# Kernel tuning notes

Hardware: AMD Instinct MI355X
Metric: run time of the kernel (lower is better)

## Reference

```python
import jax, jax.numpy as jnp
import numpy as np

N_NODES = 100000


def _graph_conv(x, src, dst, W, b):
    # DGL GraphConv, norm='both':
    # out = D_in^{-1/2} A D_out^{-1/2} x W + b, degrees clamped >= 1
    ones = jnp.ones(src.shape[0], dtype=x.dtype)
    deg_out = jax.ops.segment_sum(ones, src, num_segments=N_NODES)
    deg_in = jax.ops.segment_sum(ones, dst, num_segments=N_NODES)
    norm_src = jax.lax.rsqrt(jnp.maximum(deg_out, 1.0))  # [N]
    norm_dst = jax.lax.rsqrt(jnp.maximum(deg_in, 1.0))   # [N]
    h = x * norm_src[:, None]                    # [N, d_in]
    msg = h[src]                                 # [E, d_in] gather
    agg = jax.ops.segment_sum(msg, dst, num_segments=N_NODES)  # [N, d_in] scatter-add
    agg = agg * norm_dst[:, None]
    return agg @ W + b                           # [N, d_out]


def setup_inputs() -> dict:
    key = jax.random.key(0)
    k1, k2, k3, k4, k5 = jax.random.split(key, 5)
    n_edges = 1600000
    ndim, hdl, r = 32, 64, 32
    x = jax.random.normal(k1, (N_NODES, ndim), dtype=jnp.float32)
    src = jax.random.randint(k2, (n_edges,), 0, N_NODES, dtype=jnp.int32)
    dst = jax.random.randint(k3, (n_edges,), 0, N_NODES, dtype=jnp.int32)
    W1 = jax.random.normal(k4, (ndim, hdl), dtype=jnp.float32) / np.sqrt(ndim)
    b1 = jnp.zeros((hdl,), dtype=jnp.float32)
    W2 = jax.random.normal(k5, (hdl, r), dtype=jnp.float32) / np.sqrt(hdl)
    b2 = jnp.zeros((r,), dtype=jnp.float32)
    return {"x": x, "src": src, "dst": dst, "W1": W1, "b1": b1, "W2": W2, "b2": b2}


def reference(x, src, dst, W1, b1, W2, b2):
    z = _graph_conv(x, src, dst, W1, b1)
    z = _graph_conv(z, src, dst, W2, b2)
    return z
```

## Files before the change

### kernel.cpp

```cpp
#include <hip/hip_runtime.h>

#define N_NODES 100000
#define D_IN 32
#define D_HID 64
#define D_OUT 32
#define NBUCK 391
#define CHUNK 8192
#define CAP   8192

#define RED3(a) { a += __shfl_xor(a, 8); a += __shfl_xor(a, 16); a += __shfl_xor(a, 32); }

__global__ __launch_bounds__(256) void bucket_hist_kernel(
    const int* __restrict__ src, const int* __restrict__ dst,
    int* __restrict__ sb_cnt, int* __restrict__ db_cnt, int E) {
    __shared__ int hs[NBUCK], hd[NBUCK];
    int tid = threadIdx.x;
    for (int i = tid; i < NBUCK; i += 256) { hs[i] = 0; hd[i] = 0; }
    __syncthreads();
    int stride = gridDim.x * 256;
    for (int e = blockIdx.x * 256 + tid; e < E; e += stride) {
        atomicAdd(&hs[src[e] >> 8], 1);
        atomicAdd(&hd[dst[e] >> 8], 1);
    }
    __syncthreads();
    for (int i = tid; i < NBUCK; i += 256) {
        if (hs[i]) atomicAdd(&sb_cnt[i], hs[i]);
        if (hd[i]) atomicAdd(&db_cnt[i], hd[i]);
    }
}

__global__ __launch_bounds__(512) void bucket_scan_kernel(
    const int* __restrict__ sb_cnt, const int* __restrict__ db_cnt,
    int* __restrict__ sb_base, int* __restrict__ db_base,
    int* __restrict__ sb_cur, int* __restrict__ db_cur, int E) {
    __shared__ int s[512];
    int tid = threadIdx.x;
    int v = (tid < NBUCK) ? sb_cnt[tid] : 0;
    s[tid] = v;
    __syncthreads();
    for (int off = 1; off < 512; off <<= 1) {
        int tv = (tid >= off) ? s[tid - off] : 0;
        __syncthreads(); s[tid] += tv; __syncthreads();
    }
    if (tid < NBUCK) { int e0 = s[tid] - v; sb_base[tid] = e0; sb_cur[tid] = e0; }
    if (tid == 0) sb_base[NBUCK] = E;
    __syncthreads();
    int v2 = (tid < NBUCK) ? db_cnt[tid] : 0;
    s[tid] = v2;
    __syncthreads();
    for (int off = 1; off < 512; off <<= 1) {
        int tv = (tid >= off) ? s[tid - off] : 0;
        __syncthreads(); s[tid] += tv; __syncthreads();
    }
    if (tid < NBUCK) { int e0 = s[tid] - v2; db_base[tid] = e0; db_cur[tid] = e0; }
    if (tid == 0) db_base[NBUCK] = E;
}

__global__ __launch_bounds__(512) void partition_both_kernel(
    const int* __restrict__ src, const int* __restrict__ dst,
    int* __restrict__ sb_cur, int* __restrict__ db_cur,
    int* __restrict__ ebuf, unsigned char* __restrict__ sbuf, int E) {
    __shared__ int dh[NBUCK], sh_[NBUCK];
    __shared__ int sarr[512];
    __shared__ int dloff[NBUCK], dgb[NBUCK], dcur[NBUCK];
    __shared__ int sloff[NBUCK], sgb[NBUCK], scur[NBUCK];
    __shared__ int dbuf[CHUNK];
    __shared__ unsigned char sbytes[CHUNK];
    int tid = threadIdx.x;
    int base = blockIdx.x * CHUNK;
    int lim = E - base; if (lim > CHUNK) lim = CHUNK;

    for (int i = tid; i < NBUCK; i += 512) { dh[i] = 0; sh_[i] = 0; }
    __syncthreads();
    for (int k = tid; k < lim; k += 512) {
        atomicAdd(&dh[dst[base + k] >> 8], 1);
        atomicAdd(&sh_[src[base + k] >> 8], 1);
    }
    __syncthreads();
    int v = (tid < NBUCK) ? dh[tid] : 0;
    sarr[tid] = v;
    __syncthreads();
    for (int off = 1; off < 512; off <<= 1) {
        int tv = (tid >= off) ? sarr[tid - off] : 0;
        __syncthreads(); sarr[tid] += tv; __syncthreads();
    }
    if (tid < NBUCK) {
        int excl = sarr[tid] - v;
        dloff[tid] = excl; dcur[tid] = excl;
        dgb[tid] = v ? atomicAdd(&db_cur[tid], v) : 0;
    }
    __syncthreads();
    int v2 = (tid < NBUCK) ? sh_[tid] : 0;
    sarr[tid] = v2;
    __syncthreads();
    for (int off = 1; off < 512; off <<= 1) {
        int tv = (tid >= off) ? sarr[tid - off] : 0;
        __syncthreads(); sarr[tid] += tv; __syncthreads();
    }
    if (tid < NBUCK) {
        int excl = sarr[tid] - v2;
        sloff[tid] = excl; scur[tid] = excl;
        sgb[tid] = v2 ? atomicAdd(&sb_cur[tid], v2) : 0;
    }
    __syncthreads();
    for (int k = tid; k < lim; k += 512) {
        int d = dst[base + k], s0 = src[base + k];
        int p = atomicAdd(&dcur[d >> 8], 1);
        dbuf[p] = (s0 << 8) | (d & 255);
        int p2 = atomicAdd(&scur[s0 >> 8], 1);
        sbytes[p2] = (unsigned char)(s0 & 255);
    }
    __syncthreads();
    int w = tid >> 6, lane = tid & 63;
    for (int b = w; b < NBUCK; b += 8) {
        int st = dloff[b], len = dh[b], gb = dgb[b];
        for (int i = lane; i < len; i += 64) ebuf[gb + i] = dbuf[st + i];
        int st2 = sloff[b], len2 = sh_[b], gb2 = sgb[b];
        for (int i = lane; i < len2; i += 64) sbuf[gb2 + i] = sbytes[st2 + i];
    }
}

__global__ __launch_bounds__(256) void src_norm_prescale_kernel(
    const unsigned char* __restrict__ sbuf, const int* __restrict__ sb_base,
    const float4* __restrict__ x4, float4* __restrict__ xs4,
    float* __restrict__ norm_src, int n_nodes) {
    __shared__ int cnt[256];
    __shared__ float nsl[256];
    int b = blockIdx.x, tid = threadIdx.x;
    int st = sb_base[b], en = sb_base[b + 1];
    cnt[tid] = 0;
    __syncthreads();
    for (int k = st + tid; k < en; k += 256) atomicAdd(&cnt[sbuf[k]], 1);
    __syncthreads();
    int base_node = b << 8;
    int nn = n_nodes - base_node; if (nn > 256) nn = 256;
    if (tid < nn) {
        int d = cnt[tid];
        float ns = rsqrtf((float)(d < 1 ? 1 : d));
        norm_src[base_node + tid] = ns;
        nsl[tid] = ns;
    }
    __syncthreads();
    for (int k = tid; k < nn * 8; k += 256) {
        float4 v = x4[((long)base_node << 3) + k];
        float s = nsl[k >> 3];
        v.x *= s; v.y *= s; v.z *= s; v.w *= s;
        xs4[((long)base_node << 3) + k] = v;
    }
}

__global__ __launch_bounds__(256) void localfill_kernel(
    const int* __restrict__ ebuf, const int* __restrict__ db_base,
    int* __restrict__ rowptr, float* __restrict__ norm_dst,
    int* __restrict__ colidx, int n_nodes, int E) {
    __shared__ int limg[CAP];
    __shared__ int cnt[256];
    __shared__ int sc[256];
    int b = blockIdx.x, tid = threadIdx.x;
    int base_node = b << 8;
    int nn = n_nodes - base_node; if (nn > 256) nn = 256;
    int cbase = db_base[b], cend = db_base[b + 1];
    int len = cend - cbase;
    cnt[tid] = 0;
    __syncthreads();
    for (int k = tid; k < len; k += 256) atomicAdd(&cnt[ebuf[cbase + k] & 255], 1);
    __syncthreads();
    int v = cnt[tid];
    sc[tid] = v;
    __syncthreads();
    for (int off = 1; off < 256; off <<= 1) {
        int tv = (tid >= off) ? sc[tid - off] : 0;
        __syncthreads(); sc[tid] += tv; __syncthreads();
    }
    int excl = sc[tid] - v;
    if (tid < nn) {
        rowptr[base_node + tid] = cbase + excl;
        norm_dst[base_node + tid] = rsqrtf((float)(v < 1 ? 1 : v));
    }
    if (b == NBUCK - 1 && tid == 0) rowptr[n_nodes] = E;
    __syncthreads();
    cnt[tid] = excl;
    __syncthreads();
    if (len <= CAP) {
        for (int k = tid; k < len; k += 256) {
            int v2 = ebuf[cbase + k];
            int p = atomicAdd(&cnt[v2 & 255], 1);
            limg[p] = v2 >> 8;
        }
        __syncthreads();
        for (int k = tid; k < len; k += 256) colidx[cbase + k] = limg[k];
    } else {
        for (int k = tid; k < len; k += 256) {
            int v2 = ebuf[cbase + k];
            int p = atomicAdd(&cnt[v2 & 255], 1);
            colidx[cbase + p] = v2 >> 8;
        }
    }
}

__global__ __launch_bounds__(256) void layer1_fused(
    const float4* __restrict__ xs4, const int* __restrict__ colidx,
    const int* __restrict__ rowptr, const float* __restrict__ norm_src,
    const float* __restrict__ norm_dst,
    const float* __restrict__ W1, const float* __restrict__ b1,
    const float* __restrict__ W2, float* __restrict__ y, int n_nodes) {
    __shared__ float W1s[D_IN * D_HID];
    __shared__ float W2s[D_HID * D_OUT];
    __shared__ float b1s[D_HID];
    __shared__ float accs[4][2][D_IN];
    __shared__ float z1s[4][2][D_HID];
    int t = threadIdx.x;
    for (int i = t; i < D_IN * D_HID; i += 256) { W1s[i] = W1[i]; W2s[i] = W2[i]; }
    if (t < D_HID) b1s[t] = b1[t];
    __syncthreads();

    int w = t >> 6, lane = t & 63;
    int eh = lane >> 3;
    int q  = lane & 7;
    int j  = lane & 31;
    int half = lane >> 5;
    int npairs = (n_nodes + 1) >> 1;

    for (int p = blockIdx.x * 4 + w; p < npairs; p += gridDim.x * 4) {
        int nA = p * 2, nB = nA + 1;
        bool hasB = nB < n_nodes;
        int sA = rowptr[nA], eA = rowptr[nA + 1];
        int sB = hasB ? rowptr[nB] : 0, eB = hasB ? rowptr[nB + 1] : 0;
        int dA = eA - sA, dB = eB - sB;
        int dmax = dA > dB ? dA : dB;
        float aAx = 0.f, aAy = 0.f, aAz = 0.f, aAw = 0.f;
        float aBx = 0.f, aBy = 0.f, aBz = 0.f, aBw = 0.f;
        for (int base = 0; base < dmax; base += 64) {
            int limA = dA - base; limA = limA < 0 ? 0 : (limA > 64 ? 64 : limA);
            int limB = dB - base; limB = limB < 0 ? 0 : (limB > 64 ? 64 : limB);
            int cA = (lane < limA) ? colidx[sA + base + lane] : 0;
            int cB = (lane < limB) ? colidx[sB + base + lane] : 0;
            int lm = limA > limB ? limA : limB;
            int lim_up = (lm + 7) & ~7;
            for (int i = eh; i < lim_up; i += 8) {
                int ca = __shfl(cA, i), cb = __shfl(cB, i);
                if (i < limA) {
                    float4 v = xs4[(long)ca * 8 + q];
                    aAx += v.x; aAy += v.y; aAz += v.z; aAw += v.w;
                }
                if (i < limB) {
                    float4 v = xs4[(long)cb * 8 + q];
                    aBx += v.x; aBy += v.y; aBz += v.z; aBw += v.w;
                }
            }
        }
        RED3(aAx) RED3(aAy) RED3(aAz) RED3(aAw)
        RED3(aBx) RED3(aBy) RED3(aBz) RED3(aBw)
        if (lane < 16) {
            int s = lane >> 3, qq = lane & 7;
            accs[w][s][qq * 4 + 0] = s ? aBx : aAx;
            accs[w][s][qq * 4 + 1] = s ? aBy : aAy;
            accs[w][s][qq * 4 + 2] = s ? aBz : aAz;
            accs[w][s][qq * 4 + 3] = s ? aBw : aAw;
        }
        float ndA = norm_dst[nA], ndB = hasB ? norm_dst[nB] : 0.f;
        float s1A = 0.f, s1B = 0.f;
#pragma unroll
        for (int k = 0; k < D_IN; ++k) {
            float wv = W1s[k * D_HID + lane];
            s1A = fmaf(accs[w][0][k], wv, s1A);
            s1B = fmaf(accs[w][1][k], wv, s1B);
        }
        z1s[w][0][lane] = ndA * s1A + b1s[lane];
        z1s[w][1][lane] = ndB * s1B + b1s[lane];
        float s2 = 0.f;
#pragma unroll
        for (int k = 0; k < D_HID; ++k) s2 = fmaf(z1s[w][half][k], W2s[k * D_OUT + j], s2);
        int nn_ = half ? nB : nA;
        if (half == 0 || hasB) y[(long)nn_ * D_OUT + j] = norm_src[nn_] * s2;
    }
}

__global__ __launch_bounds__(256) void agg2_kernel(
    const float4* __restrict__ y4, const int* __restrict__ colidx,
    const int* __restrict__ rowptr, const float* __restrict__ norm_dst,
    const float* __restrict__ b2, float4* __restrict__ out4, int n_nodes) {
    int t = threadIdx.x;
    int w = t >> 6, lane = t & 63;
    int eh = lane >> 3, q = lane & 7;
    int npairs = (n_nodes + 1) >> 1;
    for (int p = blockIdx.x * 4 + w; p < npairs; p += gridDim.x * 4) {
        int nA = p * 2, nB = nA + 1;
        bool hasB = nB < n_nodes;
        int sA = rowptr[nA], eA = rowptr[nA + 1];
        int sB = hasB ? rowptr[nB] : 0, eB = hasB ? rowptr[nB + 1] : 0;
        int dA = eA - sA, dB = eB - sB;
        int dmax = dA > dB ? dA : dB;
        float aAx = 0.f, aAy = 0.f, aAz = 0.f, aAw = 0.f;
        float aBx = 0.f, aBy = 0.f, aBz = 0.f, aBw = 0.f;
        for (int base = 0; base < dmax; base += 64) {
            int limA = dA - base; limA = limA < 0 ? 0 : (limA > 64 ? 64 : limA);
            int limB = dB - base; limB = limB < 0 ? 0 : (limB > 64 ? 64 : limB);
            int cA = (lane < limA) ? colidx[sA + base + lane] : 0;
            int cB = (lane < limB) ? colidx[sB + base + lane] : 0;
            int lm = limA > limB ? limA : limB;
            int lim_up = (lm + 7) & ~7;
            for (int i = eh; i < lim_up; i += 8) {
                int ca = __shfl(cA, i), cb = __shfl(cB, i);
                if (i < limA) {
                    float4 v = y4[(long)ca * 8 + q];
                    aAx += v.x; aAy += v.y; aAz += v.z; aAw += v.w;
                }
                if (i < limB) {
                    float4 v = y4[(long)cb * 8 + q];
                    aBx += v.x; aBy += v.y; aBz += v.z; aBw += v.w;
                }
            }
        }
        RED3(aAx) RED3(aAy) RED3(aAz) RED3(aAw)
        RED3(aBx) RED3(aBy) RED3(aBz) RED3(aBw)
        if (lane < 16) {
            int s = lane >> 3;
            int nn_ = s ? nB : nA;
            if (!s || hasB) {
                float nd = norm_dst[nn_];
                const float4 bb = ((const float4*)b2)[q];
                float4 o;
                o.x = fmaf(s ? aBx : aAx, nd, bb.x);
                o.y = fmaf(s ? aBy : aAy, nd, bb.y);
                o.z = fmaf(s ? aBz : aAz, nd, bb.z);
                o.w = fmaf(s ? aBw : aAw, nd, bb.w);
                out4[(long)nn_ * 8 + q] = o;
            }
        }
    }
}

extern "C" void kernel_launch(void* const* d_in, const int* in_sizes, int n_in,
                              void* d_out, int out_size, void* d_ws, size_t ws_size,
                              hipStream_t stream) {
    const float* x   = (const float*)d_in[0];
    const int*   src = (const int*)d_in[1];
    const int*   dst = (const int*)d_in[2];
    const float* W1  = (const float*)d_in[3];
    const float* b1  = (const float*)d_in[4];
    const float* W2  = (const float*)d_in[5];
    const float* b2  = (const float*)d_in[6];

    const int N = N_NODES;
    const int E = in_sizes[1];

    int* ws_i    = (int*)d_ws;
    int* sb_cnt  = ws_i;
    int* db_cnt  = ws_i + 512;
    int* sb_base = ws_i + 1024;
    int* db_base = ws_i + 1536;
    int* sb_cur  = ws_i + 2048;
    int* db_cur  = ws_i + 2560;
    int* rowptr  = ws_i + 3072;
    int* colidx  = ws_i + 3072 + N + 4;
    float* norms = (float*)(colidx + E);
    float* yv    = norms + 2 * N;
    float* xs    = yv + 32 * N;
    int* ebuf    = (int*)yv;
    unsigned char* sbuf = (unsigned char*)(ebuf + E);

    hipMemsetAsync(ws_i, 0, 1024 * sizeof(int), stream);

    bucket_hist_kernel<<<256, 256, 0, stream>>>(src, dst, sb_cnt, db_cnt, E);
    bucket_scan_kernel<<<1, 512, 0, stream>>>(sb_cnt, db_cnt, sb_base, db_base,
                                              sb_cur, db_cur, E);

    int pb = (E + CHUNK - 1) / CHUNK;
    partition_both_kernel<<<pb, 512, 0, stream>>>(src, dst, sb_cur, db_cur,
                                                  ebuf, sbuf, E);
    src_norm_prescale_kernel<<<NBUCK, 256, 0, stream>>>(sbuf, sb_base,
                                                        (const float4*)x, (float4*)xs,
                                                        norms, N);
    localfill_kernel<<<NBUCK, 256, 0, stream>>>(ebuf, db_base, rowptr, norms + N,
                                                colidx, N, E);

    layer1_fused<<<2048, 256, 0, stream>>>((const float4*)xs, colidx, rowptr,
                                           norms, norms + N, W1, b1, W2, yv, N);
    agg2_kernel<<<2048, 256, 0, stream>>>((const float4*)yv, colidx, rowptr,
                                          norms + N, b2, (float4*)d_out, N);
}
```

Baseline: 194.7 us.

## Store gathered node features in bf16 and process one node per wavefront

The prescaled input features and the layer-1 output rows are now stored as bf16, which halves the bytes moved by the random row gathers in both aggregation kernels. Each wavefront now handles a single node with 16 edges in flight and 8 features per lane, where it previously interleaved two nodes. Rounding to bf16 adds error that may approach the correctness tolerance. The workspace layout is rearranged so the bf16 buffers alias the edge staging buffers.

```diff
diff --git a/kernel.cpp b/kernel.cpp
--- a/kernel.cpp
+++ b/kernel.cpp
@@ -8,7 +8,19 @@
 #define CHUNK 8192
 #define CAP   8192
 
-#define RED3(a) { a += __shfl_xor(a, 8); a += __shfl_xor(a, 16); a += __shfl_xor(a, 32); }
+typedef unsigned short ushort8v __attribute__((ext_vector_type(8)));
+typedef unsigned short ushort4v __attribute__((ext_vector_type(4)));
+
+__device__ __forceinline__ float bf2f(unsigned short u) {
+    return __uint_as_float((unsigned)u << 16);
+}
+__device__ __forceinline__ unsigned short f2bf(float f) {
+    unsigned u = __float_as_uint(f);
+    return (unsigned short)((u + 0x7FFF + ((u >> 16) & 1)) >> 16);
+}
+
+#define RED4(a) { a += __shfl_xor(a, 4); a += __shfl_xor(a, 8); \
+                  a += __shfl_xor(a, 16); a += __shfl_xor(a, 32); }
 
 __global__ __launch_bounds__(256) void bucket_hist_kernel(
     const int* __restrict__ src, const int* __restrict__ dst,
@@ -122,7 +134,7 @@
 
 __global__ __launch_bounds__(256) void src_norm_prescale_kernel(
     const unsigned char* __restrict__ sbuf, const int* __restrict__ sb_base,
-    const float4* __restrict__ x4, float4* __restrict__ xs4,
+    const float4* __restrict__ x4, ushort4v* __restrict__ xs4b,
     float* __restrict__ norm_src, int n_nodes) {
     __shared__ int cnt[256];
     __shared__ float nsl[256];
@@ -144,8 +156,10 @@
     for (int k = tid; k < nn * 8; k += 256) {
         float4 v = x4[((long)base_node << 3) + k];
         float s = nsl[k >> 3];
-        v.x *= s; v.y *= s; v.z *= s; v.w *= s;
-        xs4[((long)base_node << 3) + k] = v;
+        ushort4v o;
+        o[0] = f2bf(v.x * s); o[1] = f2bf(v.y * s);
+        o[2] = f2bf(v.z * s); o[3] = f2bf(v.w * s);
+        xs4b[((long)base_node << 3) + k] = o;
     }
 }
 
@@ -199,134 +213,110 @@
 }
 
 __global__ __launch_bounds__(256) void layer1_fused(
-    const float4* __restrict__ xs4, const int* __restrict__ colidx,
+    const ushort8v* __restrict__ xs8, const int* __restrict__ colidx,
     const int* __restrict__ rowptr, const float* __restrict__ norm_src,
     const float* __restrict__ norm_dst,
     const float* __restrict__ W1, const float* __restrict__ b1,
-    const float* __restrict__ W2, float* __restrict__ y, int n_nodes) {
+    const float* __restrict__ W2, unsigned short* __restrict__ ybf, int n_nodes) {
     __shared__ float W1s[D_IN * D_HID];
     __shared__ float W2s[D_HID * D_OUT];
     __shared__ float b1s[D_HID];
-    __shared__ float accs[4][2][D_IN];
-    __shared__ float z1s[4][2][D_HID];
+    __shared__ float accs[4][D_IN];
+    __shared__ float z1s[4][D_HID];
     int t = threadIdx.x;
-    for (int i = t; i < D_IN * D_HID; i += 256) { W1s[i] = W1[i]; W2s[i] = W2[i]; }
+    for (int i = t; i < 2048; i += 256) { W1s[i] = W1[i]; W2s[i] = W2[i]; }
     if (t < D_HID) b1s[t] = b1[t];
     __syncthreads();
 
     int w = t >> 6, lane = t & 63;
-    int eh = lane >> 3;
-    int q  = lane & 7;
+    int eh = lane >> 2;
+    int q  = lane & 3;
     int j  = lane & 31;
-    int half = lane >> 5;
-    int npairs = (n_nodes + 1) >> 1;
-
-    for (int p = blockIdx.x * 4 + w; p < npairs; p += gridDim.x * 4) {
-        int nA = p * 2, nB = nA + 1;
-        bool hasB = nB < n_nodes;
-        int sA = rowptr[nA], eA = rowptr[nA + 1];
-        int sB = hasB ? rowptr[nB] : 0, eB = hasB ? rowptr[nB + 1] : 0;
-        int dA = eA - sA, dB = eB - sB;
-        int dmax = dA > dB ? dA : dB;
-        float aAx = 0.f, aAy = 0.f, aAz = 0.f, aAw = 0.f;
-        float aBx = 0.f, aBy = 0.f, aBz = 0.f, aBw = 0.f;
-        for (int base = 0; base < dmax; base += 64) {
-            int limA = dA - base; limA = limA < 0 ? 0 : (limA > 64 ? 64 : limA);
-            int limB = dB - base; limB = limB < 0 ? 0 : (limB > 64 ? 64 : limB);
-            int cA = (lane < limA) ? colidx[sA + base + lane] : 0;
-            int cB = (lane < limB) ? colidx[sB + base + lane] : 0;
-            int lm = limA > limB ? limA : limB;
-            int lim_up = (lm + 7) & ~7;
-            for (int i = eh; i < lim_up; i += 8) {
-                int ca = __shfl(cA, i), cb = __shfl(cB, i);
-                if (i < limA) {
-                    float4 v = xs4[(long)ca * 8 + q];
-                    aAx += v.x; aAy += v.y; aAz += v.z; aAw += v.w;
-                }
-                if (i < limB) {
-                    float4 v = xs4[(long)cb * 8 + q];
-                    aBx += v.x; aBy += v.y; aBz += v.z; aBw += v.w;
+    int kb = (lane >> 5) * 32;
+
+    for (int n = blockIdx.x * 4 + w; n < n_nodes; n += gridDim.x * 4) {
+        int start = rowptr[n], deg = rowptr[n + 1] - start;
+        float a[8];
+#pragma unroll
+        for (int r = 0; r < 8; ++r) a[r] = 0.f;
+        for (int base = 0; base < deg; base += 64) {
+            int rem = deg - base;
+            int lim = rem < 64 ? rem : 64;
+            int lim_up = (lim + 15) & ~15;
+            int c_reg = (lane < lim) ? colidx[start + base + lane] : 0;
+            for (int i = eh; i < lim_up; i += 16) {
+                int c = __shfl(c_reg, i);
+                if (i < lim) {
+                    ushort8v v = xs8[(long)c * 4 + q];
+#pragma unroll
+                    for (int r = 0; r < 8; ++r) a[r] += bf2f(v[r]);
                 }
             }
         }
-        RED3(aAx) RED3(aAy) RED3(aAz) RED3(aAw)
-        RED3(aBx) RED3(aBy) RED3(aBz) RED3(aBw)
-        if (lane < 16) {
-            int s = lane >> 3, qq = lane & 7;
-            accs[w][s][qq * 4 + 0] = s ? aBx : aAx;
-            accs[w][s][qq * 4 + 1] = s ? aBy : aAy;
-            accs[w][s][qq * 4 + 2] = s ? aBz : aAz;
-            accs[w][s][qq * 4 + 3] = s ? aBw : aAw;
-        }
-        float ndA = norm_dst[nA], ndB = hasB ? norm_dst[nB] : 0.f;
-        float s1A = 0.f, s1B = 0.f;
-#pragma unroll
-        for (int k = 0; k < D_IN; ++k) {
-            float wv = W1s[k * D_HID + lane];
-            s1A = fmaf(accs[w][0][k], wv, s1A);
-            s1B = fmaf(accs[w][1][k], wv, s1B);
-        }
-        z1s[w][0][lane] = ndA * s1A + b1s[lane];
-        z1s[w][1][lane] = ndB * s1B + b1s[lane];
+#pragma unroll
+        for (int r = 0; r < 8; ++r) RED4(a[r])
+        if (lane < 4) {
+#pragma unroll
+            for (int r = 0; r < 8; ++r) accs[w][lane * 8 + r] = a[r];
+        }
+        float nd = norm_dst[n];
+        float s1 = 0.f;
+#pragma unroll
+        for (int k = 0; k < D_IN; ++k) s1 = fmaf(accs[w][k], W1s[k * D_HID + lane], s1);
+        z1s[w][lane] = nd * s1 + b1s[lane];
         float s2 = 0.f;
 #pragma unroll
-        for (int k = 0; k < D_HID; ++k) s2 = fmaf(z1s[w][half][k], W2s[k * D_OUT + j], s2);
-        int nn_ = half ? nB : nA;
-        if (half == 0 || hasB) y[(long)nn_ * D_OUT + j] = norm_src[nn_] * s2;
+        for (int kk = 0; kk < 32; ++kk) s2 = fmaf(z1s[w][kb + kk], W2s[(kb + kk) * D_OUT + j], s2);
+        s2 += __shfl_xor(s2, 32);
+        if (lane < 32) ybf[(long)n * D_OUT + j] = f2bf(norm_src[n] * s2);
     }
 }
 
 __global__ __launch_bounds__(256) void agg2_kernel(
-    const float4* __restrict__ y4, const int* __restrict__ colidx,
+    const ushort8v* __restrict__ y8, const int* __restrict__ colidx,
     const int* __restrict__ rowptr, const float* __restrict__ norm_dst,
-    const float* __restrict__ b2, float4* __restrict__ out4, int n_nodes) {
+    const float* __restrict__ b2, float* __restrict__ out, int n_nodes) {
+    __shared__ float b2s[D_OUT];
     int t = threadIdx.x;
+    if (t < D_OUT) b2s[t] = b2[t];
+    __syncthreads();
     int w = t >> 6, lane = t & 63;
-    int eh = lane >> 3, q = lane & 7;
-    int npairs = (n_nodes + 1) >> 1;
-    for (int p = blockIdx.x * 4 + w; p < npairs; p += gridDim.x * 4) {
-        int nA = p * 2, nB = nA + 1;
-        bool hasB = nB < n_nodes;
-        int sA = rowptr[nA], eA = rowptr[nA + 1];
-        int sB = hasB ? rowptr[nB] : 0, eB = hasB ? rowptr[nB + 1] : 0;
-        int dA = eA - sA, dB = eB - sB;
-        int dmax = dA > dB ? dA : dB;
-        float aAx = 0.f, aAy = 0.f, aAz = 0.f, aAw = 0.f;
-        float aBx = 0.f, aBy = 0.f, aBz = 0.f, aBw = 0.f;
-        for (int base = 0; base < dmax; base += 64) {
-            int limA = dA - base; limA = limA < 0 ? 0 : (limA > 64 ? 64 : limA);
-            int limB = dB - base; limB = limB < 0 ? 0 : (limB > 64 ? 64 : limB);
-            int cA = (lane < limA) ? colidx[sA + base + lane] : 0;
-            int cB = (lane < limB) ? colidx[sB + base + lane] : 0;
-            int lm = limA > limB ? limA : limB;
-            int lim_up = (lm + 7) & ~7;
-            for (int i = eh; i < lim_up; i += 8) {
-                int ca = __shfl(cA, i), cb = __shfl(cB, i);
-                if (i < limA) {
-                    float4 v = y4[(long)ca * 8 + q];
-                    aAx += v.x; aAy += v.y; aAz += v.z; aAw += v.w;
-                }
-                if (i < limB) {
-                    float4 v = y4[(long)cb * 8 + q];
-                    aBx += v.x; aBy += v.y; aBz += v.z; aBw += v.w;
+    int eh = lane >> 2, q = lane & 3;
+    for (int n = blockIdx.x * 4 + w; n < n_nodes; n += gridDim.x * 4) {
+        int start = rowptr[n], deg = rowptr[n + 1] - start;
+        float a[8];
+#pragma unroll
+        for (int r = 0; r < 8; ++r) a[r] = 0.f;
+        for (int base = 0; base < deg; base += 64) {
+            int rem = deg - base;
+            int lim = rem < 64 ? rem : 64;
+            int lim_up = (lim + 15) & ~15;
+            int c_reg = (lane < lim) ? colidx[start + base + lane] : 0;
+            for (int i = eh; i < lim_up; i += 16) {
+                int c = __shfl(c_reg, i);
+                if (i < lim) {
+                    ushort8v v = y8[(long)c * 4 + q];
+#pragma unroll
+                    for (int r = 0; r < 8; ++r) a[r] += bf2f(v[r]);
                 }
             }
         }
-        RED3(aAx) RED3(aAy) RED3(aAz) RED3(aAw)
-        RED3(aBx) RED3(aBy) RED3(aBz) RED3(aBw)
-        if (lane < 16) {
-            int s = lane >> 3;
-            int nn_ = s ? nB : nA;
-            if (!s || hasB) {
-                float nd = norm_dst[nn_];
-                const float4 bb = ((const float4*)b2)[q];
-                float4 o;
-                o.x = fmaf(s ? aBx : aAx, nd, bb.x);
-                o.y = fmaf(s ? aBy : aAy, nd, bb.y);
-                o.z = fmaf(s ? aBz : aAz, nd, bb.z);
-                o.w = fmaf(s ? aBw : aAw, nd, bb.w);
-                out4[(long)nn_ * 8 + q] = o;
-            }
+#pragma unroll
+        for (int r = 0; r < 8; ++r) RED4(a[r])
+        if (lane < 4) {
+            float nd = norm_dst[n];
+            float* orow = out + (long)n * D_OUT + lane * 8;
+            float4 o1, o2;
+            o1.x = fmaf(a[0], nd, b2s[lane * 8 + 0]);
+            o1.y = fmaf(a[1], nd, b2s[lane * 8 + 1]);
+            o1.z = fmaf(a[2], nd, b2s[lane * 8 + 2]);
+            o1.w = fmaf(a[3], nd, b2s[lane * 8 + 3]);
+            o2.x = fmaf(a[4], nd, b2s[lane * 8 + 4]);
+            o2.y = fmaf(a[5], nd, b2s[lane * 8 + 5]);
+            o2.z = fmaf(a[6], nd, b2s[lane * 8 + 6]);
+            o2.w = fmaf(a[7], nd, b2s[lane * 8 + 7]);
+            ((float4*)orow)[0] = o1;
+            ((float4*)orow)[1] = o2;
         }
     }
 }
@@ -355,10 +345,10 @@
     int* rowptr  = ws_i + 3072;
     int* colidx  = ws_i + 3072 + N + 4;
     float* norms = (float*)(colidx + E);
-    float* yv    = norms + 2 * N;
-    float* xs    = yv + 32 * N;
-    int* ebuf    = (int*)yv;
+    int* ebuf    = (int*)(norms + 2 * N);
     unsigned char* sbuf = (unsigned char*)(ebuf + E);
+    unsigned short* xsb = (unsigned short*)(sbuf + E);
+    unsigned short* ybf = (unsigned short*)ebuf;
 
     hipMemsetAsync(ws_i, 0, 1024 * sizeof(int), stream);
 
@@ -370,13 +360,13 @@
     partition_both_kernel<<<pb, 512, 0, stream>>>(src, dst, sb_cur, db_cur,
                                                   ebuf, sbuf, E);
     src_norm_prescale_kernel<<<NBUCK, 256, 0, stream>>>(sbuf, sb_base,
-                                                        (const float4*)x, (float4*)xs,
+                                                        (const float4*)x, (ushort4v*)xsb,
                                                         norms, N);
     localfill_kernel<<<NBUCK, 256, 0, stream>>>(ebuf, db_base, rowptr, norms + N,
                                                 colidx, N, E);
 
-    layer1_fused<<<2048, 256, 0, stream>>>((const float4*)xs, colidx, rowptr,
-                                           norms, norms + N, W1, b1, W2, yv, N);
-    agg2_kernel<<<2048, 256, 0, stream>>>((const float4*)yv, colidx, rowptr,
-                                          norms + N, b2, (float4*)d_out, N);
-}
+    layer1_fused<<<2048, 256, 0, stream>>>((const ushort8v*)xsb, colidx, rowptr,
+                                           norms, norms + N, W1, b1, W2, ybf, N);
+    agg2_kernel<<<2048, 256, 0, stream>>>((const ushort8v*)ybf, colidx, rowptr,
+                                          norms + N, b2, (float*)d_out, N);
+}
```

Measured after the change: 206.6 us. 1.06x slower.
